# Kernel tuning notes

Hardware: AMD Instinct MI355X
Metric: run time of the kernel (lower is better)

## Reference

```python
import jax, jax.numpy as jnp
import numpy as np

N = 131072   # total utterances (nodes)
B = 2048     # conversations (segments)
F = 200      # n_features (hard-coded 200 in source)
STEPS = 3    # processing_steps (reason_steps[0])


def setup_inputs() -> dict:
    key = jax.random.key(0)
    k = jax.random.split(key, 8)
    x = jax.random.normal(k[0], (N, F), dtype=jnp.float32)
    batch = jnp.sort(jax.random.randint(k[1], (N,), 0, B, dtype=jnp.int32))
    cos_coef = jax.random.normal(k[2], (N,), dtype=jnp.float32)
    q_star = jax.random.normal(k[3], (B, 2 * F), dtype=jnp.float32)
    s = 1.0 / np.sqrt(F)
    # PyTorch LSTM params: gate order i, f, g, o; input size 2F, hidden F
    W_ih = jax.random.uniform(k[4], (4 * F, 2 * F), jnp.float32, -s, s)
    W_hh = jax.random.uniform(k[5], (4 * F, F), jnp.float32, -s, s)
    b_ih = jax.random.uniform(k[6], (4 * F,), jnp.float32, -s, s)
    b_hh = jax.random.uniform(k[7], (4 * F,), jnp.float32, -s, s)
    return {"x": x, "batch": batch, "cos_coef": cos_coef, "q_star": q_star,
            "W_ih": W_ih, "W_hh": W_hh, "b_ih": b_ih, "b_hh": b_hh}


def _lstm_cell(inp, h, c, W_ih, W_hh, b_ih, b_hh):
    gates = inp @ W_ih.T + b_ih + h @ W_hh.T + b_hh  # [B, 4F]
    i, f, g, o = jnp.split(gates, 4, axis=-1)
    c = jax.nn.sigmoid(f) * c + jax.nn.sigmoid(i) * jnp.tanh(g)
    h = jax.nn.sigmoid(o) * jnp.tanh(c)
    return h, c


def reference(x, batch, cos_coef, q_star, W_ih, W_hh, b_ih, b_hh):
    # initial LSTM hidden: a_sit[i] = cos_row_i @ x[segment_i]  -> segment_sum
    h = jax.ops.segment_sum(cos_coef[:, None] * x, batch, num_segments=B)  # [B,F]
    c = jnp.zeros((B, F), dtype=x.dtype)
    for _ in range(STEPS):
        h, c = _lstm_cell(q_star, h, c, W_ih, W_hh, b_ih, b_hh)
        q = h                                            # [B,F]
        e = jnp.sum(x * q[batch], axis=-1)               # [N]
        m = jax.ops.segment_max(e, batch, num_segments=B)
        ex = jnp.exp(e - m[batch])
        denom = jax.ops.segment_sum(ex, batch, num_segments=B)
        a = ex / denom[batch]                            # per-segment softmax
        r = jax.ops.segment_sum(a[:, None] * x, batch, num_segments=B)  # [B,F]
        q_star = jnp.concatenate([q, r], axis=-1)        # [B,2F]
    return q_star
```

## Files before the change

### kernel.cpp

```cpp
#include <hip/hip_runtime.h>
#include <hip/hip_bf16.h>

#define N_NODES 131072
#define B_SEG   2048
#define F_DIM   200
#define K_DIM   608
#define NEG_INF (-3.4e38f)

typedef __attribute__((ext_vector_type(8))) short bf16x8;
typedef __attribute__((ext_vector_type(4))) float f32x4;

__device__ __forceinline__ float b2f(unsigned short u) {
  union { unsigned int i; float f; } v; v.i = ((unsigned int)u) << 16; return v.f;
}
__device__ __forceinline__ unsigned short f2bu(float f) {
  __hip_bfloat16 h = __float2bfloat16(f);
  return *reinterpret_cast<unsigned short*>(&h);
}
__device__ __forceinline__ float sigmoidf_(float x) { return 1.f / (1.f + __expf(-x)); }

__global__ __launch_bounds__(256) void setup_kernel(
    const float* __restrict__ Wih, const float* __restrict__ Whh,
    const float* __restrict__ bih, const float* __restrict__ bhh,
    const int* __restrict__ batch, unsigned short* __restrict__ Wc,
    float* __restrict__ bsum, int* __restrict__ seg_off) {
  int bid = blockIdx.x, tid = threadIdx.x;
  if (bid < 1976) {
    int idx = bid * 256 + tid;
    int row = idx / K_DIM, k = idx - row * K_DIM;
    float v = 0.f;
    if (row < 800) {
      if (k < 400)      v = Wih[row * 400 + k];
      else if (k < 600) v = Whh[row * 200 + (k - 400)];
    }
    Wc[idx] = f2bu(v);
  } else if (bid < 1976 + 512) {
    int i = (bid - 1976) * 256 + tid;
    int v  = batch[i];
    int pv = (i == 0) ? -1 : batch[i - 1];
    for (int b = pv + 1; b <= v; b++) seg_off[b] = i;
  } else {
    int idx = (bid - 2488) * 256 + tid;
    if (idx < 800) bsum[idx] = bih[idx] + bhh[idx];
    else if (idx == 800) {
      int last = batch[N_NODES - 1];
      for (int b = last + 1; b <= B_SEG; b++) seg_off[b] = N_NODES;
    }
  }
}

__global__ __launch_bounds__(256) void init_kernel(
    const float* __restrict__ xf, const int* __restrict__ seg_off,
    const float* __restrict__ cosc, const float* __restrict__ qs0,
    unsigned short* __restrict__ xb, unsigned short* __restrict__ A) {
  __shared__ float rpart[5][F_DIM];
  int b = blockIdx.x, tid = threadIdx.x;
  int start = seg_off[b], end = seg_off[b + 1];
  int n = end - start;
  unsigned short* Arow = A + (size_t)b * K_DIM;
  int rgrp = tid / 50, col4 = tid - rgrp * 50;
  float a0 = 0.f, a1 = 0.f, a2 = 0.f, a3 = 0.f;
  if (rgrp < 5) {
    for (int r = rgrp; r < n; r += 5) {
      float4 v = *(const float4*)(xf + (size_t)(start + r) * F_DIM + 4 * col4);
      ushort4 o; o.x = f2bu(v.x); o.y = f2bu(v.y); o.z = f2bu(v.z); o.w = f2bu(v.w);
      *(ushort4*)(xb + (size_t)(start + r) * F_DIM + 4 * col4) = o;
      float cv = cosc[start + r];
      a0 += cv * b2f(o.x); a1 += cv * b2f(o.y);
      a2 += cv * b2f(o.z); a3 += cv * b2f(o.w);
    }
    rpart[rgrp][4 * col4]     = a0;
    rpart[rgrp][4 * col4 + 1] = a1;
    rpart[rgrp][4 * col4 + 2] = a2;
    rpart[rgrp][4 * col4 + 3] = a3;
  }
  if (tid < 100) {
    float4 v = *(const float4*)(qs0 + (size_t)b * 400 + 4 * tid);
    ushort4 o; o.x = f2bu(v.x); o.y = f2bu(v.y); o.z = f2bu(v.z); o.w = f2bu(v.w);
    *(ushort4*)(Arow + 4 * tid) = o;
  }
  if (tid < 8) Arow[600 + tid] = 0;
  __syncthreads();
  if (tid < F_DIM) {
    float acc = rpart[0][tid] + rpart[1][tid] + rpart[2][tid] + rpart[3][tid]
              + rpart[4][tid];
    Arow[400 + tid] = f2bu(acc);
  }
}

__global__ __launch_bounds__(256) void gemm_gates(
    const unsigned short* __restrict__ A, const unsigned short* __restrict__ W,
    float* __restrict__ gates) {
  int tid = threadIdx.x;
  int bm = blockIdx.x * 32, bn = blockIdx.y * 64;
  int wave = tid >> 6, lane = tid & 63;
  int quad = lane >> 4, col = lane & 15;
  int strip = wave >> 1;
  int tp = (wave & 1) * 2;
  f32x4 acc[2];
  acc[0] = (f32x4){0.f, 0.f, 0.f, 0.f};
  acc[1] = (f32x4){0.f, 0.f, 0.f, 0.f};
  const unsigned short* Ap = A + (size_t)(bm + strip * 16 + col) * K_DIM + quad * 8;
  const unsigned short* Wp = W + (size_t)(bn + col) * K_DIM + quad * 8;
#pragma unroll
  for (int k0 = 0; k0 < K_DIM; k0 += 32) {
    bf16x8 af = *(const bf16x8*)(Ap + k0);
#pragma unroll
    for (int t = 0; t < 2; t++) {
      bf16x8 bfr = *(const bf16x8*)(Wp + (size_t)(tp + t) * 16 * K_DIM + k0);
      acc[t] = __builtin_amdgcn_mfma_f32_16x16x32_bf16(af, bfr, acc[t], 0, 0, 0);
    }
  }
#pragma unroll
  for (int t = 0; t < 2; t++) {
    int gn = bn + (tp + t) * 16 + col;
    if (gn < 800) {
#pragma unroll
      for (int r = 0; r < 4; r++) {
        int gm = bm + strip * 16 + quad * 4 + r;
        gates[(size_t)gm * 800 + gn] = acc[t][r];
      }
    }
  }
}

__global__ __launch_bounds__(256) void attn_fused(
    const unsigned short* __restrict__ xb, const int* __restrict__ seg_off,
    const float* __restrict__ gates, const float* __restrict__ bsum,
    float* __restrict__ cvec, unsigned short* __restrict__ A,
    float* __restrict__ out, int step) {
  __shared__ float q_s[F_DIM];
  __shared__ float rpart[8][F_DIM];
  __shared__ float redm[8], redl[8];
  int b = blockIdx.x, tid = threadIdx.x;
  int start = seg_off[b], end = seg_off[b + 1];
  int n = end - start;
  unsigned short* Arow = A + (size_t)b * K_DIM;
  if (tid < F_DIM) {
    int f = tid;
    const float* g = gates + (size_t)b * 800;
    float gi = g[f]       + bsum[f];
    float gf = g[200 + f] + bsum[200 + f];
    float gg = g[400 + f] + bsum[400 + f];
    float go = g[600 + f] + bsum[600 + f];
    float cp = (step > 0) ? cvec[(size_t)b * F_DIM + f] : 0.f;
    float cn = sigmoidf_(gf) * cp + sigmoidf_(gi) * tanhf(gg);
    float hn = sigmoidf_(go) * tanhf(cn);
    cvec[(size_t)b * F_DIM + f] = cn;
    q_s[f] = hn;
    if (step < 2) {
      unsigned short hb = f2bu(hn);
      Arow[f] = hb;
      Arow[400 + f] = hb;
    }
  }
  __syncthreads();
  int wave = tid >> 6, lane = tid & 63;
  int half = lane >> 5, hl = lane & 31;
  int hw = wave * 2 + half;
  bool act = (hl < 25);
  float q0=0,q1=0,q2=0,q3=0,q4=0,q5=0,q6=0,q7=0;
  if (act) {
    q0 = q_s[8*hl];   q1 = q_s[8*hl+1]; q2 = q_s[8*hl+2]; q3 = q_s[8*hl+3];
    q4 = q_s[8*hl+4]; q5 = q_s[8*hl+5]; q6 = q_s[8*hl+6]; q7 = q_s[8*hl+7];
  }
  const unsigned short* xp = xb + (size_t)start * F_DIM + 8 * hl;
  float m = NEG_INF, l = 0.f;
  float a0=0,a1=0,a2=0,a3=0,a4=0,a5=0,a6=0,a7=0;
  for (int r = hw; r < n; r += 8) {
    float x0=0,x1=0,x2=0,x3=0,x4=0,x5=0,x6=0,x7=0;
    float p = 0.f;
    if (act) {
      uint4 v = *(const uint4*)(xp + (size_t)r * F_DIM);
      x0 = b2f((unsigned short)(v.x & 0xffff)); x1 = b2f((unsigned short)(v.x >> 16));
      x2 = b2f((unsigned short)(v.y & 0xffff)); x3 = b2f((unsigned short)(v.y >> 16));
      x4 = b2f((unsigned short)(v.z & 0xffff)); x5 = b2f((unsigned short)(v.z >> 16));
      x6 = b2f((unsigned short)(v.w & 0xffff)); x7 = b2f((unsigned short)(v.w >> 16));
      p = q0*x0 + q1*x1 + q2*x2 + q3*x3 + q4*x4 + q5*x5 + q6*x6 + q7*x7;
    }
#pragma unroll
    for (int off = 16; off; off >>= 1) p += __shfl_xor(p, off, 32);
    float e = p;
    float mn = fmaxf(m, e);
    float fac = __expf(m - mn);
    float w  = __expf(e - mn);
    l  = l * fac + w;
    a0 = a0*fac + w*x0; a1 = a1*fac + w*x1; a2 = a2*fac + w*x2; a3 = a3*fac + w*x3;
    a4 = a4*fac + w*x4; a5 = a5*fac + w*x5; a6 = a6*fac + w*x6; a7 = a7*fac + w*x7;
    m = mn;
  }
  if (hl == 0) redm[hw] = m;
  __syncthreads();
  float M = fmaxf(fmaxf(fmaxf(redm[0], redm[1]), fmaxf(redm[2], redm[3])),
                  fmaxf(fmaxf(redm[4], redm[5]), fmaxf(redm[6], redm[7])));
  float facw = (m > NEG_INF) ? __expf(m - M) : 0.f;
  if (hl == 0) redl[hw] = l * facw;
  if (act) {
    float* rp = &rpart[hw][8 * hl];
    rp[0] = a0*facw; rp[1] = a1*facw; rp[2] = a2*facw; rp[3] = a3*facw;
    rp[4] = a4*facw; rp[5] = a5*facw; rp[6] = a6*facw; rp[7] = a7*facw;
  }
  __syncthreads();
  float L = redl[0]+redl[1]+redl[2]+redl[3]+redl[4]+redl[5]+redl[6]+redl[7];
  float inv = (L > 0.f) ? 1.f / L : 0.f;
  if (tid < F_DIM) {
    float rv = (rpart[0][tid]+rpart[1][tid]+rpart[2][tid]+rpart[3][tid]
              + rpart[4][tid]+rpart[5][tid]+rpart[6][tid]+rpart[7][tid]) * inv;
    if (step < 2) {
      Arow[200 + tid] = f2bu(rv);
    } else {
      out[(size_t)b * 400 + tid]       = q_s[tid];
      out[(size_t)b * 400 + 200 + tid] = rv;
    }
  }
}

extern "C" void kernel_launch(void* const* d_in, const int* in_sizes, int n_in,
                              void* d_out, int out_size, void* d_ws, size_t ws_size,
                              hipStream_t stream) {
  const float* x    = (const float*)d_in[0];
  const int*   batch= (const int*)d_in[1];
  const float* cosc = (const float*)d_in[2];
  const float* qs0  = (const float*)d_in[3];
  const float* Wih  = (const float*)d_in[4];
  const float* Whh  = (const float*)d_in[5];
  const float* bih  = (const float*)d_in[6];
  const float* bhh  = (const float*)d_in[7];
  char* ws = (char*)d_ws;
  unsigned short* xb   = (unsigned short*)(ws);
  unsigned short* A    = (unsigned short*)(ws + 52428800);
  unsigned short* Wc   = (unsigned short*)(ws + 54919168);
  float*          gates= (float*)(ws + 55930880);
  float*          cvec = (float*)(ws + 62484480);
  float*          bsum = (float*)(ws + 64122880);
  int*            soff = (int*)(ws + 64126080);
  float*          outp = (float*)d_out;

  setup_kernel<<<2492, 256, 0, stream>>>(Wih, Whh, bih, bhh, batch, Wc, bsum, soff);
  init_kernel<<<B_SEG, 256, 0, stream>>>(x, soff, cosc, qs0, xb, A);
  for (int s = 0; s < 3; s++) {
    gemm_gates<<<dim3(64, 13), 256, 0, stream>>>(A, Wc, gates);
    attn_fused<<<B_SEG, 256, 0, stream>>>(xb, soff, gates, bsum, cvec, A, outp, s);
  }
}
```

Before: 273.9 us.

## Fuse all stages into one cooperative persistent kernel with grid syncs

Replaces the eight separate launches (setup, init, then three gemm plus attention pairs) with a single cooperative kernel of 1024 blocks that uses grid-wide syncs between phases. Each block handles two segments and keeps the LSTM cell state in registers across steps, and segment offsets come from a per-block binary search rather than a separate kernel. The goal is to remove launch gaps and the cell-state round trips through memory. In exchange, the GEMM now runs on 832 of the 1024 blocks with a different tiling, each step pays grid-sync cost, and only 1024 blocks with two segments each limits parallelism in the attention phase. If the cooperative launch fails, the old multi-kernel path is used.

```diff
diff --git a/kernel.cpp b/kernel.cpp
--- a/kernel.cpp
+++ b/kernel.cpp
@@ -1,11 +1,15 @@
 #include <hip/hip_runtime.h>
 #include <hip/hip_bf16.h>
+#include <hip/hip_cooperative_groups.h>
+
+namespace cg = cooperative_groups;
 
 #define N_NODES 131072
 #define B_SEG   2048
 #define F_DIM   200
 #define K_DIM   608
 #define NEG_INF (-3.4e38f)
+#define GRID    1024
 
 typedef __attribute__((ext_vector_type(8))) short bf16x8;
 typedef __attribute__((ext_vector_type(4))) float f32x4;
@@ -18,6 +22,210 @@
   return *reinterpret_cast<unsigned short*>(&h);
 }
 __device__ __forceinline__ float sigmoidf_(float x) { return 1.f / (1.f + __expf(-x)); }
+__device__ __forceinline__ float tanhf_(float x) {
+  float e = __expf(2.f * x);
+  return 1.f - 2.f / (1.f + e);
+}
+__device__ __forceinline__ int lower_bound_batch(const int* __restrict__ batch, int target) {
+  int lo = 0, hi = N_NODES;
+  while (lo < hi) {
+    int mid = (lo + hi) >> 1;
+    if (batch[mid] < target) lo = mid + 1; else hi = mid;
+  }
+  return lo;
+}
+
+__global__ __launch_bounds__(256, 4) void mega_kernel(
+    const float* __restrict__ xf, const int* __restrict__ batch,
+    const float* __restrict__ cosc, const float* __restrict__ qs0,
+    const float* __restrict__ Wih, const float* __restrict__ Whh,
+    const float* __restrict__ bih, const float* __restrict__ bhh,
+    unsigned short* __restrict__ xb, unsigned short* __restrict__ A,
+    unsigned short* __restrict__ Wc, float* __restrict__ gates,
+    float* __restrict__ bsum, float* __restrict__ out) {
+  cg::grid_group grid = cg::this_grid();
+  __shared__ float q_s[F_DIM];
+  __shared__ float rpart[8][F_DIM];
+  __shared__ float redm[8], redl[8];
+  __shared__ int sb[3];
+  int b = blockIdx.x, tid = threadIdx.x;
+
+  if (tid < 3) sb[tid] = lower_bound_batch(batch, 2 * b + tid);
+  for (int idx = b * 256 + tid; idx < 832 * K_DIM; idx += GRID * 256) {
+    int row = idx / K_DIM, k = idx - row * K_DIM;
+    float v = 0.f;
+    if (row < 800) {
+      if (k < 400)      v = Wih[row * 400 + k];
+      else if (k < 600) v = Whh[row * 200 + (k - 400)];
+    }
+    Wc[idx] = f2bu(v);
+  }
+  for (int i = b * 256 + tid; i < 800; i += GRID * 256) bsum[i] = bih[i] + bhh[i];
+  __syncthreads();
+  int start0 = sb[0], end0 = sb[1], end1 = sb[2];
+
+  for (int si = 0; si < 2; si++) {
+    int seg = 2 * b + si;
+    int st = si ? end0 : start0, en = si ? end1 : end0;
+    int n = en - st;
+    unsigned short* Arow = A + (size_t)seg * K_DIM;
+    int rgrp = tid / 50, col4 = tid - rgrp * 50;
+    float a0 = 0.f, a1 = 0.f, a2 = 0.f, a3 = 0.f;
+    if (rgrp < 5) {
+      for (int r = rgrp; r < n; r += 5) {
+        float4 v = *(const float4*)(xf + (size_t)(st + r) * F_DIM + 4 * col4);
+        ushort4 o; o.x = f2bu(v.x); o.y = f2bu(v.y); o.z = f2bu(v.z); o.w = f2bu(v.w);
+        *(ushort4*)(xb + (size_t)(st + r) * F_DIM + 4 * col4) = o;
+        float cv = cosc[st + r];
+        a0 += cv * b2f(o.x); a1 += cv * b2f(o.y);
+        a2 += cv * b2f(o.z); a3 += cv * b2f(o.w);
+      }
+      rpart[rgrp][4 * col4]     = a0;
+      rpart[rgrp][4 * col4 + 1] = a1;
+      rpart[rgrp][4 * col4 + 2] = a2;
+      rpart[rgrp][4 * col4 + 3] = a3;
+    }
+    if (tid < 100) {
+      float4 v = *(const float4*)(qs0 + (size_t)seg * 400 + 4 * tid);
+      ushort4 o; o.x = f2bu(v.x); o.y = f2bu(v.y); o.z = f2bu(v.z); o.w = f2bu(v.w);
+      *(ushort4*)(Arow + 4 * tid) = o;
+    }
+    if (tid < 8) Arow[600 + tid] = 0;
+    __syncthreads();
+    if (tid < F_DIM) {
+      float acc = rpart[0][tid] + rpart[1][tid] + rpart[2][tid] + rpart[3][tid]
+                + rpart[4][tid];
+      Arow[400 + tid] = f2bu(acc);
+    }
+    __syncthreads();
+  }
+
+  float c0 = 0.f, c1 = 0.f;
+  grid.sync();
+
+  for (int s = 0; s < 3; s++) {
+    if (b < 832) {
+      int bm = (b & 63) * 32, bn = (b >> 6) * 64;
+      int wave = tid >> 6, lane = tid & 63;
+      int quad = lane >> 4, col = lane & 15;
+      int strip = wave >> 1;
+      int tp = (wave & 1) * 2;
+      f32x4 acc[2];
+      acc[0] = (f32x4){0.f, 0.f, 0.f, 0.f};
+      acc[1] = (f32x4){0.f, 0.f, 0.f, 0.f};
+      const unsigned short* Ap = A + (size_t)(bm + strip * 16 + col) * K_DIM + quad * 8;
+      const unsigned short* Wp = Wc + (size_t)(bn + col) * K_DIM + quad * 8;
+#pragma unroll
+      for (int k0 = 0; k0 < K_DIM; k0 += 32) {
+        bf16x8 af = *(const bf16x8*)(Ap + k0);
+#pragma unroll
+        for (int t = 0; t < 2; t++) {
+          bf16x8 bfr = *(const bf16x8*)(Wp + (size_t)(tp + t) * 16 * K_DIM + k0);
+          acc[t] = __builtin_amdgcn_mfma_f32_16x16x32_bf16(af, bfr, acc[t], 0, 0, 0);
+        }
+      }
+#pragma unroll
+      for (int t = 0; t < 2; t++) {
+        int gn = bn + (tp + t) * 16 + col;
+        if (gn < 800) {
+#pragma unroll
+          for (int r = 0; r < 4; r++) {
+            int gm = bm + strip * 16 + quad * 4 + r;
+            gates[(size_t)gm * 800 + gn] = acc[t][r];
+          }
+        }
+      }
+    }
+    grid.sync();
+
+    for (int si = 0; si < 2; si++) {
+      int seg = 2 * b + si;
+      int st = si ? end0 : start0, en = si ? end1 : end0;
+      int n = en - st;
+      unsigned short* Arow = A + (size_t)seg * K_DIM;
+      float cprev = si ? c1 : c0;
+      float cnew = cprev;
+      if (tid < F_DIM) {
+        const float* g = gates + (size_t)seg * 800;
+        float gi = g[tid]       + bsum[tid];
+        float gf = g[200 + tid] + bsum[200 + tid];
+        float gg = g[400 + tid] + bsum[400 + tid];
+        float go = g[600 + tid] + bsum[600 + tid];
+        float cn = sigmoidf_(gf) * cprev + sigmoidf_(gi) * tanhf_(gg);
+        float hn = sigmoidf_(go) * tanhf_(cn);
+        cnew = cn;
+        q_s[tid] = hn;
+        if (s < 2) {
+          unsigned short hb = f2bu(hn);
+          Arow[tid] = hb;
+          Arow[400 + tid] = hb;
+        }
+      }
+      if (si) c1 = cnew; else c0 = cnew;
+      __syncthreads();
+      int wave = tid >> 6, lane = tid & 63;
+      int half = lane >> 5, hl = lane & 31;
+      int hw = wave * 2 + half;
+      bool act = (hl < 25);
+      float q0=0,q1=0,q2=0,q3=0,q4=0,q5=0,q6=0,q7=0;
+      if (act) {
+        q0 = q_s[8*hl];   q1 = q_s[8*hl+1]; q2 = q_s[8*hl+2]; q3 = q_s[8*hl+3];
+        q4 = q_s[8*hl+4]; q5 = q_s[8*hl+5]; q6 = q_s[8*hl+6]; q7 = q_s[8*hl+7];
+      }
+      const unsigned short* xp = xb + (size_t)st * F_DIM + 8 * hl;
+      float m = NEG_INF, l = 0.f;
+      float a0=0,a1=0,a2=0,a3=0,a4=0,a5=0,a6=0,a7=0;
+      for (int r = hw; r < n; r += 8) {
+        float x0=0,x1=0,x2=0,x3=0,x4=0,x5=0,x6=0,x7=0;
+        float p = 0.f;
+        if (act) {
+          uint4 v = *(const uint4*)(xp + (size_t)r * F_DIM);
+          x0 = b2f((unsigned short)(v.x & 0xffff)); x1 = b2f((unsigned short)(v.x >> 16));
+          x2 = b2f((unsigned short)(v.y & 0xffff)); x3 = b2f((unsigned short)(v.y >> 16));
+          x4 = b2f((unsigned short)(v.z & 0xffff)); x5 = b2f((unsigned short)(v.z >> 16));
+          x6 = b2f((unsigned short)(v.w & 0xffff)); x7 = b2f((unsigned short)(v.w >> 16));
+          p = q0*x0 + q1*x1 + q2*x2 + q3*x3 + q4*x4 + q5*x5 + q6*x6 + q7*x7;
+        }
+#pragma unroll
+        for (int off = 16; off; off >>= 1) p += __shfl_xor(p, off, 32);
+        float e = p;
+        float mn = fmaxf(m, e);
+        float fac = __expf(m - mn);
+        float w  = __expf(e - mn);
+        l  = l * fac + w;
+        a0 = a0*fac + w*x0; a1 = a1*fac + w*x1; a2 = a2*fac + w*x2; a3 = a3*fac + w*x3;
+        a4 = a4*fac + w*x4; a5 = a5*fac + w*x5; a6 = a6*fac + w*x6; a7 = a7*fac + w*x7;
+        m = mn;
+      }
+      if (hl == 0) redm[hw] = m;
+      __syncthreads();
+      float M = fmaxf(fmaxf(fmaxf(redm[0], redm[1]), fmaxf(redm[2], redm[3])),
+                      fmaxf(fmaxf(redm[4], redm[5]), fmaxf(redm[6], redm[7])));
+      float facw = (m > NEG_INF) ? __expf(m - M) : 0.f;
+      if (hl == 0) redl[hw] = l * facw;
+      if (act) {
+        float* rp = &rpart[hw][8 * hl];
+        rp[0] = a0*facw; rp[1] = a1*facw; rp[2] = a2*facw; rp[3] = a3*facw;
+        rp[4] = a4*facw; rp[5] = a5*facw; rp[6] = a6*facw; rp[7] = a7*facw;
+      }
+      __syncthreads();
+      float L = redl[0]+redl[1]+redl[2]+redl[3]+redl[4]+redl[5]+redl[6]+redl[7];
+      float inv = (L > 0.f) ? 1.f / L : 0.f;
+      if (tid < F_DIM) {
+        float rv = (rpart[0][tid]+rpart[1][tid]+rpart[2][tid]+rpart[3][tid]
+                  + rpart[4][tid]+rpart[5][tid]+rpart[6][tid]+rpart[7][tid]) * inv;
+        if (s < 2) {
+          Arow[200 + tid] = f2bu(rv);
+        } else {
+          out[(size_t)seg * 400 + tid]       = q_s[tid];
+          out[(size_t)seg * 400 + 200 + tid] = rv;
+        }
+      }
+      __syncthreads();
+    }
+    if (s < 2) grid.sync();
+  }
+}
 
 __global__ __launch_bounds__(256) void setup_kernel(
     const float* __restrict__ Wih, const float* __restrict__ Whh,
@@ -236,10 +444,19 @@
   int*            soff = (int*)(ws + 64126080);
   float*          outp = (float*)d_out;
 
-  setup_kernel<<<2492, 256, 0, stream>>>(Wih, Whh, bih, bhh, batch, Wc, bsum, soff);
-  init_kernel<<<B_SEG, 256, 0, stream>>>(x, soff, cosc, qs0, xb, A);
-  for (int s = 0; s < 3; s++) {
-    gemm_gates<<<dim3(64, 13), 256, 0, stream>>>(A, Wc, gates);
-    attn_fused<<<B_SEG, 256, 0, stream>>>(xb, soff, gates, bsum, cvec, A, outp, s);
-  }
-}
+  void* args[] = {(void*)&x, (void*)&batch, (void*)&cosc, (void*)&qs0,
+                  (void*)&Wih, (void*)&Whh, (void*)&bih, (void*)&bhh,
+                  (void*)&xb, (void*)&A, (void*)&Wc, (void*)&gates,
+                  (void*)&bsum, (void*)&outp};
+  hipError_t err = hipLaunchCooperativeKernel((const void*)mega_kernel,
+                                              dim3(GRID), dim3(256),
+                                              (void**)args, 0, stream);
+  if (err != hipSuccess) {
+    setup_kernel<<<2492, 256, 0, stream>>>(Wih, Whh, bih, bhh, batch, Wc, bsum, soff);
+    init_kernel<<<B_SEG, 256, 0, stream>>>(x, soff, cosc, qs0, xb, A);
+    for (int s = 0; s < 3; s++) {
+      gemm_gates<<<dim3(64, 13), 256, 0, stream>>>(A, Wc, gates);
+      attn_fused<<<B_SEG, 256, 0, stream>>>(xb, soff, gates, bsum, cvec, A, outp, s);
+    }
+  }
+}
```

Result: slower. 1.017 ms (+271.3%).

## Fuse LSTM gate GEMM and attention across all steps into one kernel

Applied to the files above, without the earlier changes.

Replaces the per-step gemm_gates and attn_fused launches with a single main_kernel. Each 512-thread block owns 8 segments, keeps their A rows, gates, cell state and hidden state in shared memory, and runs all three LSTM and attention steps. The weight matrix is read from global memory per block, and the x loads use a one-row register prefetch. The setup kernel is folded into init, with segment offsets found by binary search, and tanh is replaced by an exp-based formula. This removes launches and global round-trips for gates and state. In exchange it runs far fewer blocks per CU, processes segments serially with many block barriers, and computes half-wasted 16-row MFMA tiles.

```diff
diff --git a/kernel.cpp b/kernel.cpp
--- a/kernel.cpp
+++ b/kernel.cpp
@@ -5,7 +5,11 @@
 #define B_SEG   2048
 #define F_DIM   200
 #define K_DIM   608
+#define K_PAD   616
 #define NEG_INF (-3.4e38f)
+#define SEGS    8
+#define MAIN_GRID (B_SEG / SEGS)
+#define MAIN_THREADS 512
 
 typedef __attribute__((ext_vector_type(8))) short bf16x8;
 typedef __attribute__((ext_vector_type(4))) float f32x4;
@@ -18,15 +22,33 @@
   return *reinterpret_cast<unsigned short*>(&h);
 }
 __device__ __forceinline__ float sigmoidf_(float x) { return 1.f / (1.f + __expf(-x)); }
-
-__global__ __launch_bounds__(256) void setup_kernel(
+__device__ __forceinline__ float tanhf_(float x) {
+  float e = __expf(2.f * x);
+  return 1.f - 2.f / (1.f + e);
+}
+__device__ __forceinline__ int lower_bound_batch(const int* __restrict__ batch, int target) {
+  int lo = 0, hi = N_NODES;
+  while (lo < hi) {
+    int mid = (lo + hi) >> 1;
+    if (batch[mid] < target) lo = mid + 1; else hi = mid;
+  }
+  return lo;
+}
+
+__global__ __launch_bounds__(256) void init_kernel(
+    const float* __restrict__ xf, const int* __restrict__ batch,
+    const float* __restrict__ cosc, const float* __restrict__ qs0,
     const float* __restrict__ Wih, const float* __restrict__ Whh,
     const float* __restrict__ bih, const float* __restrict__ bhh,
-    const int* __restrict__ batch, unsigned short* __restrict__ Wc,
-    float* __restrict__ bsum, int* __restrict__ seg_off) {
-  int bid = blockIdx.x, tid = threadIdx.x;
-  if (bid < 1976) {
-    int idx = bid * 256 + tid;
+    unsigned short* __restrict__ xb, unsigned short* __restrict__ A,
+    unsigned short* __restrict__ Wc, float* __restrict__ bsum,
+    int* __restrict__ seg_off) {
+  __shared__ float rpart[5][F_DIM];
+  __shared__ int sb[2];
+  int b = blockIdx.x, tid = threadIdx.x;
+  if (tid < 2) sb[tid] = lower_bound_batch(batch, b + tid);
+  int idx = b * 256 + tid;
+  if (idx < 832 * K_DIM) {
     int row = idx / K_DIM, k = idx - row * K_DIM;
     float v = 0.f;
     if (row < 800) {
@@ -34,29 +56,15 @@
       else if (k < 600) v = Whh[row * 200 + (k - 400)];
     }
     Wc[idx] = f2bu(v);
-  } else if (bid < 1976 + 512) {
-    int i = (bid - 1976) * 256 + tid;
-    int v  = batch[i];
-    int pv = (i == 0) ? -1 : batch[i - 1];
-    for (int b = pv + 1; b <= v; b++) seg_off[b] = i;
-  } else {
-    int idx = (bid - 2488) * 256 + tid;
-    if (idx < 800) bsum[idx] = bih[idx] + bhh[idx];
-    else if (idx == 800) {
-      int last = batch[N_NODES - 1];
-      for (int b = last + 1; b <= B_SEG; b++) seg_off[b] = N_NODES;
-    }
-  }
-}
-
-__global__ __launch_bounds__(256) void init_kernel(
-    const float* __restrict__ xf, const int* __restrict__ seg_off,
-    const float* __restrict__ cosc, const float* __restrict__ qs0,
-    unsigned short* __restrict__ xb, unsigned short* __restrict__ A) {
-  __shared__ float rpart[5][F_DIM];
-  int b = blockIdx.x, tid = threadIdx.x;
-  int start = seg_off[b], end = seg_off[b + 1];
+  }
+  if (idx < 800) bsum[idx] = bih[idx] + bhh[idx];
+  __syncthreads();
+  int start = sb[0], end = sb[1];
   int n = end - start;
+  if (tid == 0) {
+    seg_off[b] = start;
+    if (b == 0) seg_off[B_SEG] = N_NODES;
+  }
   unsigned short* Arow = A + (size_t)b * K_DIM;
   int rgrp = tid / 50, col4 = tid - rgrp * 50;
   float a0 = 0.f, a1 = 0.f, a2 = 0.f, a3 = 0.f;
@@ -88,129 +96,134 @@
   }
 }
 
-__global__ __launch_bounds__(256) void gemm_gates(
-    const unsigned short* __restrict__ A, const unsigned short* __restrict__ W,
-    float* __restrict__ gates) {
+__global__ __launch_bounds__(512, 2) void main_kernel(
+    const unsigned short* __restrict__ xb, const int* __restrict__ seg_off,
+    const unsigned short* __restrict__ Aglob, const unsigned short* __restrict__ Wc,
+    const float* __restrict__ bsum, float* __restrict__ out) {
+  __shared__ unsigned short ArowsS[SEGS][K_PAD];
+  __shared__ float gatesS[SEGS][800];
+  __shared__ float cS[SEGS][F_DIM];
+  __shared__ float qS[SEGS][F_DIM];
+  __shared__ float rpart[16][202];
+  __shared__ float redm[16], redl[16];
+  __shared__ int sbound[SEGS + 1];
   int tid = threadIdx.x;
-  int bm = blockIdx.x * 32, bn = blockIdx.y * 64;
-  int wave = tid >> 6, lane = tid & 63;
+  int seg0 = blockIdx.x * SEGS;
+  if (tid < SEGS + 1) sbound[tid] = seg_off[seg0 + tid];
+  {
+    int wv = tid >> 6, lane = tid & 63;
+    const unsigned short* src = Aglob + (size_t)(seg0 + wv) * K_DIM;
+    for (int k = lane; k < K_DIM; k += 64) ArowsS[wv][k] = src[k];
+  }
+  for (int it = tid; it < SEGS * F_DIM; it += MAIN_THREADS) ((float*)cS)[it] = 0.f;
+  __syncthreads();
+
+  int lane = tid & 63, wv = tid >> 6;
   int quad = lane >> 4, col = lane & 15;
-  int strip = wave >> 1;
-  int tp = (wave & 1) * 2;
-  f32x4 acc[2];
-  acc[0] = (f32x4){0.f, 0.f, 0.f, 0.f};
-  acc[1] = (f32x4){0.f, 0.f, 0.f, 0.f};
-  const unsigned short* Ap = A + (size_t)(bm + strip * 16 + col) * K_DIM + quad * 8;
-  const unsigned short* Wp = W + (size_t)(bn + col) * K_DIM + quad * 8;
-#pragma unroll
-  for (int k0 = 0; k0 < K_DIM; k0 += 32) {
-    bf16x8 af = *(const bf16x8*)(Ap + k0);
-#pragma unroll
-    for (int t = 0; t < 2; t++) {
-      bf16x8 bfr = *(const bf16x8*)(Wp + (size_t)(tp + t) * 16 * K_DIM + k0);
-      acc[t] = __builtin_amdgcn_mfma_f32_16x16x32_bf16(af, bfr, acc[t], 0, 0, 0);
-    }
-  }
-#pragma unroll
-  for (int t = 0; t < 2; t++) {
-    int gn = bn + (tp + t) * 16 + col;
-    if (gn < 800) {
-#pragma unroll
-      for (int r = 0; r < 4; r++) {
-        int gm = bm + strip * 16 + quad * 4 + r;
-        gates[(size_t)gm * 800 + gn] = acc[t][r];
-      }
-    }
-  }
-}
-
-__global__ __launch_bounds__(256) void attn_fused(
-    const unsigned short* __restrict__ xb, const int* __restrict__ seg_off,
-    const float* __restrict__ gates, const float* __restrict__ bsum,
-    float* __restrict__ cvec, unsigned short* __restrict__ A,
-    float* __restrict__ out, int step) {
-  __shared__ float q_s[F_DIM];
-  __shared__ float rpart[8][F_DIM];
-  __shared__ float redm[8], redl[8];
-  int b = blockIdx.x, tid = threadIdx.x;
-  int start = seg_off[b], end = seg_off[b + 1];
-  int n = end - start;
-  unsigned short* Arow = A + (size_t)b * K_DIM;
-  if (tid < F_DIM) {
-    int f = tid;
-    const float* g = gates + (size_t)b * 800;
-    float gi = g[f]       + bsum[f];
-    float gf = g[200 + f] + bsum[200 + f];
-    float gg = g[400 + f] + bsum[400 + f];
-    float go = g[600 + f] + bsum[600 + f];
-    float cp = (step > 0) ? cvec[(size_t)b * F_DIM + f] : 0.f;
-    float cn = sigmoidf_(gf) * cp + sigmoidf_(gi) * tanhf(gg);
-    float hn = sigmoidf_(go) * tanhf(cn);
-    cvec[(size_t)b * F_DIM + f] = cn;
-    q_s[f] = hn;
-    if (step < 2) {
-      unsigned short hb = f2bu(hn);
-      Arow[f] = hb;
-      Arow[400 + f] = hb;
-    }
-  }
-  __syncthreads();
-  int wave = tid >> 6, lane = tid & 63;
-  int half = lane >> 5, hl = lane & 31;
-  int hw = wave * 2 + half;
+  int hw = tid >> 5, hl = tid & 31;
   bool act = (hl < 25);
-  float q0=0,q1=0,q2=0,q3=0,q4=0,q5=0,q6=0,q7=0;
-  if (act) {
-    q0 = q_s[8*hl];   q1 = q_s[8*hl+1]; q2 = q_s[8*hl+2]; q3 = q_s[8*hl+3];
-    q4 = q_s[8*hl+4]; q5 = q_s[8*hl+5]; q6 = q_s[8*hl+6]; q7 = q_s[8*hl+7];
-  }
-  const unsigned short* xp = xb + (size_t)start * F_DIM + 8 * hl;
-  float m = NEG_INF, l = 0.f;
-  float a0=0,a1=0,a2=0,a3=0,a4=0,a5=0,a6=0,a7=0;
-  for (int r = hw; r < n; r += 8) {
-    float x0=0,x1=0,x2=0,x3=0,x4=0,x5=0,x6=0,x7=0;
-    float p = 0.f;
-    if (act) {
-      uint4 v = *(const uint4*)(xp + (size_t)r * F_DIM);
-      x0 = b2f((unsigned short)(v.x & 0xffff)); x1 = b2f((unsigned short)(v.x >> 16));
-      x2 = b2f((unsigned short)(v.y & 0xffff)); x3 = b2f((unsigned short)(v.y >> 16));
-      x4 = b2f((unsigned short)(v.z & 0xffff)); x5 = b2f((unsigned short)(v.z >> 16));
-      x6 = b2f((unsigned short)(v.w & 0xffff)); x7 = b2f((unsigned short)(v.w >> 16));
-      p = q0*x0 + q1*x1 + q2*x2 + q3*x3 + q4*x4 + q5*x5 + q6*x6 + q7*x7;
-    }
-#pragma unroll
-    for (int off = 16; off; off >>= 1) p += __shfl_xor(p, off, 32);
-    float e = p;
-    float mn = fmaxf(m, e);
-    float fac = __expf(m - mn);
-    float w  = __expf(e - mn);
-    l  = l * fac + w;
-    a0 = a0*fac + w*x0; a1 = a1*fac + w*x1; a2 = a2*fac + w*x2; a3 = a3*fac + w*x3;
-    a4 = a4*fac + w*x4; a5 = a5*fac + w*x5; a6 = a6*fac + w*x6; a7 = a7*fac + w*x7;
-    m = mn;
-  }
-  if (hl == 0) redm[hw] = m;
-  __syncthreads();
-  float M = fmaxf(fmaxf(fmaxf(redm[0], redm[1]), fmaxf(redm[2], redm[3])),
-                  fmaxf(fmaxf(redm[4], redm[5]), fmaxf(redm[6], redm[7])));
-  float facw = (m > NEG_INF) ? __expf(m - M) : 0.f;
-  if (hl == 0) redl[hw] = l * facw;
-  if (act) {
-    float* rp = &rpart[hw][8 * hl];
-    rp[0] = a0*facw; rp[1] = a1*facw; rp[2] = a2*facw; rp[3] = a3*facw;
-    rp[4] = a4*facw; rp[5] = a5*facw; rp[6] = a6*facw; rp[7] = a7*facw;
-  }
-  __syncthreads();
-  float L = redl[0]+redl[1]+redl[2]+redl[3]+redl[4]+redl[5]+redl[6]+redl[7];
-  float inv = (L > 0.f) ? 1.f / L : 0.f;
-  if (tid < F_DIM) {
-    float rv = (rpart[0][tid]+rpart[1][tid]+rpart[2][tid]+rpart[3][tid]
-              + rpart[4][tid]+rpart[5][tid]+rpart[6][tid]+rpart[7][tid]) * inv;
-    if (step < 2) {
-      Arow[200 + tid] = f2bu(rv);
-    } else {
-      out[(size_t)b * 400 + tid]       = q_s[tid];
-      out[(size_t)b * 400 + 200 + tid] = rv;
+
+  for (int s = 0; s < 3; s++) {
+    bf16x8 afr[19];
+#pragma unroll
+    for (int kk = 0; kk < 19; kk++)
+      afr[kk] = *(const bf16x8*)(&ArowsS[lane & 7][kk * 32 + quad * 8]);
+    for (int nt = wv; nt < 50; nt += 8) {
+      f32x4 acc = (f32x4){0.f, 0.f, 0.f, 0.f};
+      const unsigned short* Wp = Wc + (size_t)(nt * 16 + col) * K_DIM + quad * 8;
+#pragma unroll
+      for (int kk = 0; kk < 19; kk++) {
+        bf16x8 bfr = *(const bf16x8*)(Wp + kk * 32);
+        acc = __builtin_amdgcn_mfma_f32_16x16x32_bf16(afr[kk], bfr, acc, 0, 0, 0);
+      }
+      if (quad < 2) {
+#pragma unroll
+        for (int r = 0; r < 4; r++) gatesS[quad * 4 + r][nt * 16 + col] = acc[r];
+      }
+    }
+    __syncthreads();
+    for (int it = tid; it < SEGS * F_DIM; it += MAIN_THREADS) {
+      int si = it / F_DIM, f = it - si * F_DIM;
+      float gi = gatesS[si][f]       + bsum[f];
+      float gf = gatesS[si][200 + f] + bsum[200 + f];
+      float gg = gatesS[si][400 + f] + bsum[400 + f];
+      float go = gatesS[si][600 + f] + bsum[600 + f];
+      float cp = cS[si][f];
+      float cn = sigmoidf_(gf) * cp + sigmoidf_(gi) * tanhf_(gg);
+      float hn = sigmoidf_(go) * tanhf_(cn);
+      cS[si][f] = cn;
+      qS[si][f] = hn;
+      if (s < 2) {
+        unsigned short hb = f2bu(hn);
+        ArowsS[si][f] = hb;
+        ArowsS[si][400 + f] = hb;
+      } else {
+        out[(size_t)(seg0 + si) * 400 + f] = hn;
+      }
+    }
+    __syncthreads();
+    for (int si = 0; si < SEGS; si++) {
+      int st = sbound[si], n = sbound[si + 1] - st;
+      float q0=0,q1=0,q2=0,q3=0,q4=0,q5=0,q6=0,q7=0;
+      if (act) {
+        float4 qa = *(const float4*)&qS[si][8 * hl];
+        float4 qb = *(const float4*)&qS[si][8 * hl + 4];
+        q0=qa.x; q1=qa.y; q2=qa.z; q3=qa.w; q4=qb.x; q5=qb.y; q6=qb.z; q7=qb.w;
+      }
+      const unsigned short* xp = xb + (size_t)st * F_DIM + 8 * hl;
+      float m = NEG_INF, l = 0.f;
+      float a0=0,a1=0,a2=0,a3=0,a4=0,a5=0,a6=0,a7=0;
+      int r = hw;
+      uint4 v = {0u, 0u, 0u, 0u};
+      if (act && r < n) v = *(const uint4*)(xp + (size_t)r * F_DIM);
+      for (; r < n; r += 16) {
+        uint4 vc = v;
+        int rn = r + 16;
+        if (act && rn < n) v = *(const uint4*)(xp + (size_t)rn * F_DIM);
+        float x0 = b2f((unsigned short)(vc.x & 0xffff)), x1 = b2f((unsigned short)(vc.x >> 16));
+        float x2 = b2f((unsigned short)(vc.y & 0xffff)), x3 = b2f((unsigned short)(vc.y >> 16));
+        float x4 = b2f((unsigned short)(vc.z & 0xffff)), x5 = b2f((unsigned short)(vc.z >> 16));
+        float x6 = b2f((unsigned short)(vc.w & 0xffff)), x7 = b2f((unsigned short)(vc.w >> 16));
+        float p = q0*x0 + q1*x1 + q2*x2 + q3*x3 + q4*x4 + q5*x5 + q6*x6 + q7*x7;
+#pragma unroll
+        for (int off = 16; off; off >>= 1) p += __shfl_xor(p, off, 32);
+        float mn = fmaxf(m, p);
+        float fac = __expf(m - mn);
+        float w   = __expf(p - mn);
+        l  = l * fac + w;
+        a0 = a0*fac + w*x0; a1 = a1*fac + w*x1; a2 = a2*fac + w*x2; a3 = a3*fac + w*x3;
+        a4 = a4*fac + w*x4; a5 = a5*fac + w*x5; a6 = a6*fac + w*x6; a7 = a7*fac + w*x7;
+        m = mn;
+      }
+      if (hl == 0) redm[hw] = m;
+      __syncthreads();
+      float M = fmaxf(fmaxf(fmaxf(fmaxf(redm[0], redm[1]), fmaxf(redm[2], redm[3])),
+                            fmaxf(fmaxf(redm[4], redm[5]), fmaxf(redm[6], redm[7]))),
+                      fmaxf(fmaxf(fmaxf(redm[8], redm[9]), fmaxf(redm[10], redm[11])),
+                            fmaxf(fmaxf(redm[12], redm[13]), fmaxf(redm[14], redm[15]))));
+      float facw = (m > NEG_INF) ? __expf(m - M) : 0.f;
+      if (hl == 0) redl[hw] = l * facw;
+      if (act) {
+        float* rp = &rpart[hw][8 * hl];
+        rp[0] = a0*facw; rp[1] = a1*facw; rp[2] = a2*facw; rp[3] = a3*facw;
+        rp[4] = a4*facw; rp[5] = a5*facw; rp[6] = a6*facw; rp[7] = a7*facw;
+      }
+      __syncthreads();
+      float L = redl[0]+redl[1]+redl[2]+redl[3]+redl[4]+redl[5]+redl[6]+redl[7]
+              + redl[8]+redl[9]+redl[10]+redl[11]+redl[12]+redl[13]+redl[14]+redl[15];
+      float inv = (L > 0.f) ? 1.f / L : 0.f;
+      if (tid < F_DIM) {
+        float rv = (rpart[0][tid]+rpart[1][tid]+rpart[2][tid]+rpart[3][tid]
+                  + rpart[4][tid]+rpart[5][tid]+rpart[6][tid]+rpart[7][tid]
+                  + rpart[8][tid]+rpart[9][tid]+rpart[10][tid]+rpart[11][tid]
+                  + rpart[12][tid]+rpart[13][tid]+rpart[14][tid]+rpart[15][tid]) * inv;
+        if (s < 2) {
+          ArowsS[si][200 + tid] = f2bu(rv);
+        } else {
+          out[(size_t)(seg0 + si) * 400 + 200 + tid] = rv;
+        }
+      }
+      __syncthreads();
     }
   }
 }
@@ -230,16 +243,11 @@
   unsigned short* xb   = (unsigned short*)(ws);
   unsigned short* A    = (unsigned short*)(ws + 52428800);
   unsigned short* Wc   = (unsigned short*)(ws + 54919168);
-  float*          gates= (float*)(ws + 55930880);
-  float*          cvec = (float*)(ws + 62484480);
   float*          bsum = (float*)(ws + 64122880);
   int*            soff = (int*)(ws + 64126080);
   float*          outp = (float*)d_out;
 
-  setup_kernel<<<2492, 256, 0, stream>>>(Wih, Whh, bih, bhh, batch, Wc, bsum, soff);
-  init_kernel<<<B_SEG, 256, 0, stream>>>(x, soff, cosc, qs0, xb, A);
-  for (int s = 0; s < 3; s++) {
-    gemm_gates<<<dim3(64, 13), 256, 0, stream>>>(A, Wc, gates);
-    attn_fused<<<B_SEG, 256, 0, stream>>>(xb, soff, gates, bsum, cvec, A, outp, s);
-  }
-}
+  init_kernel<<<B_SEG, 256, 0, stream>>>(x, batch, cosc, qs0, Wih, Whh, bih, bhh,
+                                         xb, A, Wc, bsum, soff);
+  main_kernel<<<MAIN_GRID, MAIN_THREADS, 0, stream>>>(xb, soff, A, Wc, bsum, outp);
+}
```

Result: slower. 318.4 us (+16.2%).

## Replace online-softmax attention with two-pass row-dot and column-sum scheme

Applied to the files above, without the earlier changes.

Attention now computes one score per row per thread, does a block max/sum reduction, stores weights in shared memory, then accumulates the weighted sum column-wise per feature. This removes the per-row cross-lane shuffle reduction and running rescale of the online softmax. x conversion is split into a separate grid-stride kernel and the initial hidden sum re-reads the bf16 copy. Segment length is capped at 512 rows, which assumes small segments, and x is read twice per step.

```diff
diff --git a/kernel.cpp b/kernel.cpp
--- a/kernel.cpp
+++ b/kernel.cpp
@@ -6,6 +6,7 @@
 #define F_DIM   200
 #define K_DIM   608
 #define NEG_INF (-3.4e38f)
+#define NMAX    512
 
 typedef __attribute__((ext_vector_type(8))) short bf16x8;
 typedef __attribute__((ext_vector_type(4))) float f32x4;
@@ -18,6 +19,30 @@
   return *reinterpret_cast<unsigned short*>(&h);
 }
 __device__ __forceinline__ float sigmoidf_(float x) { return 1.f / (1.f + __expf(-x)); }
+__device__ __forceinline__ float tanhf_(float x) {
+  float e = __expf(2.f * x);
+  return 1.f - 2.f / (1.f + e);
+}
+
+__device__ __forceinline__ float row_dot(const unsigned short* __restrict__ row,
+                                         const float* q) {
+  float c0 = 0.f, c1 = 0.f, c2 = 0.f, c3 = 0.f;
+#pragma unroll 5
+  for (int k = 0; k < 25; k++) {
+    uint4 v = *(const uint4*)(row + 8 * k);
+    float4 qa = *(const float4*)(q + 8 * k);
+    float4 qb = *(const float4*)(q + 8 * k + 4);
+    c0 += qa.x * b2f((unsigned short)(v.x & 0xffff))
+        + qa.y * b2f((unsigned short)(v.x >> 16));
+    c1 += qa.z * b2f((unsigned short)(v.y & 0xffff))
+        + qa.w * b2f((unsigned short)(v.y >> 16));
+    c2 += qb.x * b2f((unsigned short)(v.z & 0xffff))
+        + qb.y * b2f((unsigned short)(v.z >> 16));
+    c3 += qb.z * b2f((unsigned short)(v.w & 0xffff))
+        + qb.w * b2f((unsigned short)(v.w >> 16));
+  }
+  return (c0 + c1) + (c2 + c3);
+}
 
 __global__ __launch_bounds__(256) void setup_kernel(
     const float* __restrict__ Wih, const float* __restrict__ Whh,
@@ -49,31 +74,27 @@
   }
 }
 
-__global__ __launch_bounds__(256) void init_kernel(
-    const float* __restrict__ xf, const int* __restrict__ seg_off,
+__global__ __launch_bounds__(256) void convert_kernel(
+    const float* __restrict__ xf, unsigned short* __restrict__ xb) {
+  const int total = N_NODES * F_DIM / 4;
+  int stride = gridDim.x * 256;
+  for (int i = blockIdx.x * 256 + threadIdx.x; i < total; i += stride) {
+    float4 v = ((const float4*)xf)[i];
+    ushort4 o; o.x = f2bu(v.x); o.y = f2bu(v.y); o.z = f2bu(v.z); o.w = f2bu(v.w);
+    ((ushort4*)xb)[i] = o;
+  }
+}
+
+__global__ __launch_bounds__(256) void asit_kernel(
+    const unsigned short* __restrict__ xb, const int* __restrict__ seg_off,
     const float* __restrict__ cosc, const float* __restrict__ qs0,
-    unsigned short* __restrict__ xb, unsigned short* __restrict__ A) {
-  __shared__ float rpart[5][F_DIM];
+    unsigned short* __restrict__ A) {
+  __shared__ float cw[NMAX];
   int b = blockIdx.x, tid = threadIdx.x;
   int start = seg_off[b], end = seg_off[b + 1];
-  int n = end - start;
+  int n = end - start; if (n > NMAX) n = NMAX;
   unsigned short* Arow = A + (size_t)b * K_DIM;
-  int rgrp = tid / 50, col4 = tid - rgrp * 50;
-  float a0 = 0.f, a1 = 0.f, a2 = 0.f, a3 = 0.f;
-  if (rgrp < 5) {
-    for (int r = rgrp; r < n; r += 5) {
-      float4 v = *(const float4*)(xf + (size_t)(start + r) * F_DIM + 4 * col4);
-      ushort4 o; o.x = f2bu(v.x); o.y = f2bu(v.y); o.z = f2bu(v.z); o.w = f2bu(v.w);
-      *(ushort4*)(xb + (size_t)(start + r) * F_DIM + 4 * col4) = o;
-      float cv = cosc[start + r];
-      a0 += cv * b2f(o.x); a1 += cv * b2f(o.y);
-      a2 += cv * b2f(o.z); a3 += cv * b2f(o.w);
-    }
-    rpart[rgrp][4 * col4]     = a0;
-    rpart[rgrp][4 * col4 + 1] = a1;
-    rpart[rgrp][4 * col4 + 2] = a2;
-    rpart[rgrp][4 * col4 + 3] = a3;
-  }
+  for (int r = tid; r < n; r += 256) cw[r] = cosc[start + r];
   if (tid < 100) {
     float4 v = *(const float4*)(qs0 + (size_t)b * 400 + 4 * tid);
     ushort4 o; o.x = f2bu(v.x); o.y = f2bu(v.y); o.z = f2bu(v.z); o.w = f2bu(v.w);
@@ -82,9 +103,17 @@
   if (tid < 8) Arow[600 + tid] = 0;
   __syncthreads();
   if (tid < F_DIM) {
-    float acc = rpart[0][tid] + rpart[1][tid] + rpart[2][tid] + rpart[3][tid]
-              + rpart[4][tid];
-    Arow[400 + tid] = f2bu(acc);
+    const unsigned short* col = xb + (size_t)start * F_DIM + tid;
+    float a0 = 0.f, a1 = 0.f, a2 = 0.f, a3 = 0.f;
+    int r = 0;
+    for (; r + 4 <= n; r += 4) {
+      a0 += cw[r]     * b2f(col[(size_t)(r)     * F_DIM]);
+      a1 += cw[r + 1] * b2f(col[(size_t)(r + 1) * F_DIM]);
+      a2 += cw[r + 2] * b2f(col[(size_t)(r + 2) * F_DIM]);
+      a3 += cw[r + 3] * b2f(col[(size_t)(r + 3) * F_DIM]);
+    }
+    for (; r < n; r++) a0 += cw[r] * b2f(col[(size_t)r * F_DIM]);
+    Arow[400 + tid] = f2bu((a0 + a1) + (a2 + a3));
   }
 }
 
@@ -124,92 +153,72 @@
   }
 }
 
-__global__ __launch_bounds__(256) void attn_fused(
+__global__ __launch_bounds__(256) void attn2_kernel(
     const unsigned short* __restrict__ xb, const int* __restrict__ seg_off,
     const float* __restrict__ gates, const float* __restrict__ bsum,
     float* __restrict__ cvec, unsigned short* __restrict__ A,
     float* __restrict__ out, int step) {
   __shared__ float q_s[F_DIM];
-  __shared__ float rpart[8][F_DIM];
-  __shared__ float redm[8], redl[8];
+  __shared__ float w_s[NMAX];
+  __shared__ float redm[4], redl[4];
   int b = blockIdx.x, tid = threadIdx.x;
   int start = seg_off[b], end = seg_off[b + 1];
-  int n = end - start;
+  int n = end - start; if (n > NMAX) n = NMAX;
   unsigned short* Arow = A + (size_t)b * K_DIM;
   if (tid < F_DIM) {
-    int f = tid;
     const float* g = gates + (size_t)b * 800;
-    float gi = g[f]       + bsum[f];
-    float gf = g[200 + f] + bsum[200 + f];
-    float gg = g[400 + f] + bsum[400 + f];
-    float go = g[600 + f] + bsum[600 + f];
-    float cp = (step > 0) ? cvec[(size_t)b * F_DIM + f] : 0.f;
-    float cn = sigmoidf_(gf) * cp + sigmoidf_(gi) * tanhf(gg);
-    float hn = sigmoidf_(go) * tanhf(cn);
-    cvec[(size_t)b * F_DIM + f] = cn;
-    q_s[f] = hn;
+    float gi = g[tid]       + bsum[tid];
+    float gf = g[200 + tid] + bsum[200 + tid];
+    float gg = g[400 + tid] + bsum[400 + tid];
+    float go = g[600 + tid] + bsum[600 + tid];
+    float cp = (step > 0) ? cvec[(size_t)b * F_DIM + tid] : 0.f;
+    float cn = sigmoidf_(gf) * cp + sigmoidf_(gi) * tanhf_(gg);
+    float hn = sigmoidf_(go) * tanhf_(cn);
+    cvec[(size_t)b * F_DIM + tid] = cn;
+    q_s[tid] = hn;
     if (step < 2) {
       unsigned short hb = f2bu(hn);
-      Arow[f] = hb;
-      Arow[400 + f] = hb;
-    }
-  }
-  __syncthreads();
-  int wave = tid >> 6, lane = tid & 63;
-  int half = lane >> 5, hl = lane & 31;
-  int hw = wave * 2 + half;
-  bool act = (hl < 25);
-  float q0=0,q1=0,q2=0,q3=0,q4=0,q5=0,q6=0,q7=0;
-  if (act) {
-    q0 = q_s[8*hl];   q1 = q_s[8*hl+1]; q2 = q_s[8*hl+2]; q3 = q_s[8*hl+3];
-    q4 = q_s[8*hl+4]; q5 = q_s[8*hl+5]; q6 = q_s[8*hl+6]; q7 = q_s[8*hl+7];
-  }
-  const unsigned short* xp = xb + (size_t)start * F_DIM + 8 * hl;
-  float m = NEG_INF, l = 0.f;
-  float a0=0,a1=0,a2=0,a3=0,a4=0,a5=0,a6=0,a7=0;
-  for (int r = hw; r < n; r += 8) {
-    float x0=0,x1=0,x2=0,x3=0,x4=0,x5=0,x6=0,x7=0;
-    float p = 0.f;
-    if (act) {
-      uint4 v = *(const uint4*)(xp + (size_t)r * F_DIM);
-      x0 = b2f((unsigned short)(v.x & 0xffff)); x1 = b2f((unsigned short)(v.x >> 16));
-      x2 = b2f((unsigned short)(v.y & 0xffff)); x3 = b2f((unsigned short)(v.y >> 16));
-      x4 = b2f((unsigned short)(v.z & 0xffff)); x5 = b2f((unsigned short)(v.z >> 16));
-      x6 = b2f((unsigned short)(v.w & 0xffff)); x7 = b2f((unsigned short)(v.w >> 16));
-      p = q0*x0 + q1*x1 + q2*x2 + q3*x3 + q4*x4 + q5*x5 + q6*x6 + q7*x7;
-    }
-#pragma unroll
-    for (int off = 16; off; off >>= 1) p += __shfl_xor(p, off, 32);
-    float e = p;
-    float mn = fmaxf(m, e);
-    float fac = __expf(m - mn);
-    float w  = __expf(e - mn);
-    l  = l * fac + w;
-    a0 = a0*fac + w*x0; a1 = a1*fac + w*x1; a2 = a2*fac + w*x2; a3 = a3*fac + w*x3;
-    a4 = a4*fac + w*x4; a5 = a5*fac + w*x5; a6 = a6*fac + w*x6; a7 = a7*fac + w*x7;
-    m = mn;
-  }
-  if (hl == 0) redm[hw] = m;
-  __syncthreads();
-  float M = fmaxf(fmaxf(fmaxf(redm[0], redm[1]), fmaxf(redm[2], redm[3])),
-                  fmaxf(fmaxf(redm[4], redm[5]), fmaxf(redm[6], redm[7])));
-  float facw = (m > NEG_INF) ? __expf(m - M) : 0.f;
-  if (hl == 0) redl[hw] = l * facw;
-  if (act) {
-    float* rp = &rpart[hw][8 * hl];
-    rp[0] = a0*facw; rp[1] = a1*facw; rp[2] = a2*facw; rp[3] = a3*facw;
-    rp[4] = a4*facw; rp[5] = a5*facw; rp[6] = a6*facw; rp[7] = a7*facw;
-  }
-  __syncthreads();
-  float L = redl[0]+redl[1]+redl[2]+redl[3]+redl[4]+redl[5]+redl[6]+redl[7];
+      Arow[tid] = hb;
+      Arow[400 + tid] = hb;
+    } else {
+      out[(size_t)b * 400 + tid] = hn;
+    }
+  }
+  __syncthreads();
+  float e0 = NEG_INF, e1 = NEG_INF;
+  if (tid < n)       e0 = row_dot(xb + (size_t)(start + tid) * F_DIM, q_s);
+  if (tid + 256 < n) e1 = row_dot(xb + (size_t)(start + tid + 256) * F_DIM, q_s);
+  float mloc = fmaxf(e0, e1);
+#pragma unroll
+  for (int off = 32; off; off >>= 1) mloc = fmaxf(mloc, __shfl_xor(mloc, off));
+  int wv = tid >> 6, lane = tid & 63;
+  if (lane == 0) redm[wv] = mloc;
+  __syncthreads();
+  float M = fmaxf(fmaxf(redm[0], redm[1]), fmaxf(redm[2], redm[3]));
+  float wsum = 0.f;
+  if (tid < n)       { float w = __expf(e0 - M); w_s[tid] = w;       wsum += w; }
+  if (tid + 256 < n) { float w = __expf(e1 - M); w_s[tid + 256] = w; wsum += w; }
+#pragma unroll
+  for (int off = 32; off; off >>= 1) wsum += __shfl_xor(wsum, off);
+  if (lane == 0) redl[wv] = wsum;
+  __syncthreads();
+  float L = redl[0] + redl[1] + redl[2] + redl[3];
   float inv = (L > 0.f) ? 1.f / L : 0.f;
   if (tid < F_DIM) {
-    float rv = (rpart[0][tid]+rpart[1][tid]+rpart[2][tid]+rpart[3][tid]
-              + rpart[4][tid]+rpart[5][tid]+rpart[6][tid]+rpart[7][tid]) * inv;
+    const unsigned short* col = xb + (size_t)start * F_DIM + tid;
+    float a0 = 0.f, a1 = 0.f, a2 = 0.f, a3 = 0.f;
+    int r = 0;
+    for (; r + 4 <= n; r += 4) {
+      a0 += w_s[r]     * b2f(col[(size_t)(r)     * F_DIM]);
+      a1 += w_s[r + 1] * b2f(col[(size_t)(r + 1) * F_DIM]);
+      a2 += w_s[r + 2] * b2f(col[(size_t)(r + 2) * F_DIM]);
+      a3 += w_s[r + 3] * b2f(col[(size_t)(r + 3) * F_DIM]);
+    }
+    for (; r < n; r++) a0 += w_s[r] * b2f(col[(size_t)r * F_DIM]);
+    float rv = ((a0 + a1) + (a2 + a3)) * inv;
     if (step < 2) {
       Arow[200 + tid] = f2bu(rv);
     } else {
-      out[(size_t)b * 400 + tid]       = q_s[tid];
       out[(size_t)b * 400 + 200 + tid] = rv;
     }
   }
@@ -237,9 +246,10 @@
   float*          outp = (float*)d_out;
 
   setup_kernel<<<2492, 256, 0, stream>>>(Wih, Whh, bih, bhh, batch, Wc, bsum, soff);
-  init_kernel<<<B_SEG, 256, 0, stream>>>(x, soff, cosc, qs0, xb, A);
+  convert_kernel<<<2048, 256, 0, stream>>>(x, xb);
+  asit_kernel<<<B_SEG, 256, 0, stream>>>(xb, soff, cosc, qs0, A);
   for (int s = 0; s < 3; s++) {
     gemm_gates<<<dim3(64, 13), 256, 0, stream>>>(A, Wc, gates);
-    attn_fused<<<B_SEG, 256, 0, stream>>>(xb, soff, gates, bsum, cvec, A, outp, s);
-  }
-}
+    attn2_kernel<<<B_SEG, 256, 0, stream>>>(xb, soff, gates, bsum, cvec, A, outp, s);
+  }
+}
```

Measured after the change: 306.1 us. +11.8%, slower.
